# Performance work log

Hardware: AMD Instinct MI355X
Metric: run time of the kernel (lower is better)

## Reference

```python
import jax, jax.numpy as jnp
import numpy as np

D_MODEL = 1024
N_HEADS = 16
HEAD_DIM = D_MODEL // N_HEADS
B, T = 2, 2048

def setup_inputs() -> dict:
    key = jax.random.key(0)
    ks = jax.random.split(key, 9)
    s = 1.0 / np.sqrt(D_MODEL)
    return {
        "x": jax.random.normal(ks[0], (B, T, D_MODEL), dtype=jnp.float32),
        "Wq": jax.random.normal(ks[1], (D_MODEL, D_MODEL), dtype=jnp.float32) * s,
        "bq": jax.random.normal(ks[2], (D_MODEL,), dtype=jnp.float32) * 0.01,
        "Wk": jax.random.normal(ks[3], (D_MODEL, D_MODEL), dtype=jnp.float32) * s,
        "bk": jax.random.normal(ks[4], (D_MODEL,), dtype=jnp.float32) * 0.01,
        "Wv": jax.random.normal(ks[5], (D_MODEL, D_MODEL), dtype=jnp.float32) * s,
        "bv": jax.random.normal(ks[6], (D_MODEL,), dtype=jnp.float32) * 0.01,
        "Wo": jax.random.normal(ks[7], (D_MODEL, D_MODEL), dtype=jnp.float32) * s,
        "bo": jax.random.normal(ks[8], (D_MODEL,), dtype=jnp.float32) * 0.01,
    }

def reference(x, Wq, bq, Wk, bk, Wv, bv, Wo, bo):
    b, t, c = x.shape
    # Projections; reshape to [B, H, T, Dh]
    def heads(w, bias):
        return (x @ w.T + bias).reshape(b, t, N_HEADS, HEAD_DIM).transpose(0, 2, 1, 3)
    q = heads(Wq, bq)
    k = heads(Wk, bk)
    v = heads(Wv, bv)
    scale = 1.0 / np.sqrt(HEAD_DIM)
    att = jnp.einsum("bhqd,bhkd->bhqk", q, k) * scale  # [B,H,T,T]
    causal = jnp.tril(jnp.ones((t, t), dtype=bool))
    att = jnp.where(causal, att, -jnp.inf)
    att = jax.nn.softmax(att, axis=-1)
    # dropout p=0.0 (eval) -> identity
    y = jnp.einsum("bhqk,bhkd->bhqd", att, v)  # [B,H,T,Dh]
    y = y.transpose(0, 2, 1, 3).reshape(b, t, c)
    return y @ Wo.T + bo
```

## Files before the change

kernel.cpp:

```cpp
#include <hip/hip_runtime.h>
#include <stdint.h>


typedef unsigned short u16;
typedef __attribute__((ext_vector_type(8)))  __bf16 bf16x8;
typedef __attribute__((ext_vector_type(4)))  float  f32x4;
typedef __attribute__((ext_vector_type(16))) float  f32x16;
typedef __attribute__((ext_vector_type(4)))  float  float4v;
typedef __attribute__((ext_vector_type(4)))  unsigned short u16x4;
typedef __attribute__((ext_vector_type(4)))  unsigned int   u32x4;
typedef __attribute__((ext_vector_type(8)))  short  short8;

#define BB 2
#define TT 2048
#define DD 1024
#define HH 16
#define DH 64
#define MM (BB*TT)
#define NSLOT 1280
#define CEXP 0.18033688011f
#define XNE ((size_t)MM*DD)
#define WNE ((size_t)DD*DD)

static __device__ __forceinline__ u16 f2bf(float f) {
    uint32_t u = __builtin_bit_cast(uint32_t, f);
    u += 0x7FFFu + ((u >> 16) & 1u);
    return (u16)(u >> 16);
}
static __device__ __forceinline__ float bf2f(u16 v) {
    uint32_t u = (uint32_t)v << 16;
    return __builtin_bit_cast(float, u);
}

static __device__ __forceinline__ unsigned cvt_pk_bf16(float a, float b) {
    unsigned r;
    asm("v_cvt_pk_bf16_f32 %0, %1, %2" : "=v"(r) : "v"(a), "v"(b));
    return r;
}

static __device__ __forceinline__ void load_lds16(const u16* g, const u16* lds_base) {
    __builtin_amdgcn_global_load_lds(
        (const __attribute__((address_space(1))) void*)(uintptr_t)g,
        (__attribute__((address_space(3)))  void*)(uint32_t)(uintptr_t)lds_base,
        16u, 0, 0u);
}

static __device__ __forceinline__ f32x4 mfma16(bf16x8 a, bf16x8 b, f32x4 c) {
    return __builtin_amdgcn_mfma_f32_16x16x32_bf16(a, b, c, 0, 0, 0);
}
static __device__ __forceinline__ f32x16 mfma32(bf16x8 a, bf16x8 b, f32x16 c) {
    return __builtin_amdgcn_mfma_f32_32x32x16_bf16(a, b, c, 0, 0, 0);
}

static __device__ __forceinline__ float tree_sum16(const f32x16& a) {
    float m[8];
#pragma unroll
    for (int r = 0; r < 8; ++r) m[r] = a[r] + a[r + 8];
#pragma unroll
    for (int off = 4; off; off >>= 1)
#pragma unroll
        for (int r = 0; r < off; ++r) m[r] += m[r + off];
    return m[0];
}

static __device__ __forceinline__ bf16x8 pack8(float s0, float s1, float s2,
        float s3, float s4, float s5, float s6, float s7) {
    unsigned c0 = cvt_pk_bf16(s0, s1);
    unsigned c1 = cvt_pk_bf16(s2, s3);
    unsigned c2 = cvt_pk_bf16(s4, s5);
    unsigned c3 = cvt_pk_bf16(s6, s7);
    asm volatile("v_permlane32_swap_b32 %0, %1" : "+v"(c0), "+v"(c2));
    asm volatile("v_permlane32_swap_b32 %0, %1" : "+v"(c1), "+v"(c3));
    u32x4 w; w[0] = c0; w[1] = c1; w[2] = c2; w[3] = c3;
    return __builtin_bit_cast(bf16x8, w);
}

__global__ __launch_bounds__(256) void cvt_kernel(const float* __restrict__ src,
                                                  u16* __restrict__ dst, int n8) {
    int i = blockIdx.x * blockDim.x + threadIdx.x;
    int stride = gridDim.x * blockDim.x;
    for (; i < n8; i += stride) {
        float4v a = ((const float4v*)src)[2 * i];
        float4v b = ((const float4v*)src)[2 * i + 1];
        u32x4 o;
        o[0] = cvt_pk_bf16(a[0], a[1]); o[1] = cvt_pk_bf16(a[2], a[3]);
        o[2] = cvt_pk_bf16(b[0], b[1]); o[3] = cvt_pk_bf16(b[2], b[3]);
        ((u32x4*)dst)[i] = o;
    }
}

__global__ __launch_bounds__(256) void cvt4_kernel(const float* __restrict__ s0,
        const float* __restrict__ s1, const float* __restrict__ s2,
        const float* __restrict__ s3, u16* __restrict__ d0, u16* __restrict__ d1,
        u16* __restrict__ d2, u16* __restrict__ d3, int n8) {
    const int z = blockIdx.y;
    const float* src = (z == 0) ? s0 : (z == 1) ? s1 : (z == 2) ? s2 : s3;
    u16* dst = (z == 0) ? d0 : (z == 1) ? d1 : (z == 2) ? d2 : d3;
    const float sc = (z == 0) ? CEXP : 1.0f;
    int i = blockIdx.x * blockDim.x + threadIdx.x;
    int stride = gridDim.x * blockDim.x;
    for (; i < n8; i += stride) {
        float4v a = ((const float4v*)src)[2 * i];
        float4v b = ((const float4v*)src)[2 * i + 1];
        u32x4 o;
        o[0] = cvt_pk_bf16(a[0] * sc, a[1] * sc);
        o[1] = cvt_pk_bf16(a[2] * sc, a[3] * sc);
        o[2] = cvt_pk_bf16(b[0] * sc, b[1] * sc);
        o[3] = cvt_pk_bf16(b[2] * sc, b[3] * sc);
        ((u32x4*)dst)[i] = o;
    }
}

template<int MODE>
__global__ __launch_bounds__(256) void gemm2(const u16* __restrict__ xb,
        const u16* __restrict__ Wb, const float* __restrict__ bq,
        const float* __restrict__ bk, const float* __restrict__ bvv,
        u16* __restrict__ outq, u16* __restrict__ vt, float* __restrict__ outf) {
    __shared__ alignas(16) u16 As[2][128 * 32];
    __shared__ alignas(16) u16 Bs[2][128 * 32];

    const int tid  = threadIdx.x;
    const int wave = tid >> 6, lane = tid & 63;
    const int lr = lane & 15, lg = lane >> 4;
    const int wr = wave >> 1, wc = wave & 1;
    const int K = 1024;

    const u16 *Ap, *Wp;
    int m0, n0, zb = 0;
    bool vtmode = false;
    const int id = blockIdx.x;
    if (MODE == 0) {
        if (id < 512) {
            zb = id >> 8; int r = id & 255;
            m0 = (r >> 3) * 128; n0 = (r & 7) * 128;
            Ap = xb; Wp = Wb + (size_t)zb * WNE;
        } else {
            int v = id - 512; zb = v >> 7; int r = v & 127;
            m0 = (r >> 4) * 128; n0 = (r & 15) * 128;
            Ap = Wb + 2 * WNE;
            Wp = xb + (size_t)zb * 2048 * 1024;
            vtmode = true;
        }
    } else {
        m0 = (id >> 3) * 128; n0 = (id & 7) * 128;
        Ap = xb; Wp = Wb;
    }

    f32x4 acc[4][4];
#pragma unroll
    for (int m = 0; m < 4; ++m)
#pragma unroll
        for (int n = 0; n < 4; ++n) acc[m][n] = (f32x4){0.f, 0.f, 0.f, 0.f};

#define G_STAGE(BB_, KK_)                                                     \
    {                                                                         \
        _Pragma("unroll")                                                     \
        for (int it = 0; it < 2; ++it) {                                      \
            int c = it * 256 + tid;                                           \
            int row = c >> 2, cc = (c & 3) * 8;                               \
            load_lds16(Ap + (size_t)(m0 + row) * K + (KK_) + cc,              \
                       &As[BB_][(size_t)(it * 256 + wave * 64) * 8]);         \
            load_lds16(Wp + (size_t)(n0 + row) * K + (KK_) + cc,              \
                       &Bs[BB_][(size_t)(it * 256 + wave * 64) * 8]);         \
        }                                                                     \
    }

    G_STAGE(0, 0);
    __syncthreads();
    int cur = 0;
    for (int k0 = 0; k0 < K; k0 += 32) {
        if (k0 + 32 < K) G_STAGE(cur ^ 1, k0 + 32);

        bf16x8 af[4], bfm[4];
#pragma unroll
        for (int m = 0; m < 4; ++m)
            af[m] = *(const bf16x8*)&As[cur][(wr * 64 + m * 16 + lr) * 32 + lg * 8];
#pragma unroll
        for (int n = 0; n < 4; ++n)
            bfm[n] = *(const bf16x8*)&Bs[cur][(wc * 64 + n * 16 + lr) * 32 + lg * 8];
#pragma unroll
        for (int m = 0; m < 4; ++m)
#pragma unroll
            for (int n = 0; n < 4; ++n)
                acc[m][n] = mfma16(af[m], bfm[n], acc[m][n]);

        __syncthreads();
        cur ^= 1;
    }
#undef G_STAGE

    if (MODE == 1) {
#pragma unroll
        for (int n = 0; n < 4; ++n) {
            int col = n0 + wc * 64 + n * 16 + lr;
            float bvl = bq[col];
#pragma unroll
            for (int m = 0; m < 4; ++m) {
                int row = m0 + wr * 64 + m * 16 + lg * 4;
#pragma unroll
                for (int r = 0; r < 4; ++r)
                    outf[(size_t)(row + r) * 1024 + col] = acc[m][n][r] + bvl;
            }
        }
    } else if (!vtmode) {
        const float* bias = zb ? bk : bq;
        const float bsc = zb ? 1.0f : CEXP;
#pragma unroll
        for (int n = 0; n < 4; ++n) {
            int col = n0 + wc * 64 + n * 16 + lr;
            float bvl = bias[col] * bsc;
#pragma unroll
            for (int m = 0; m < 4; ++m) {
                int row = m0 + wr * 64 + m * 16 + lg * 4;
#pragma unroll
                for (int r = 0; r < 4; ++r)
                    outq[(size_t)zb * XNE + (size_t)(row + r) * 1024 + col] =
                        f2bf(acc[m][n][r] + bvl);
            }
        }
    } else {
        u16* vo = vt + (size_t)zb * 1024 * 2048;
#pragma unroll
        for (int m = 0; m < 4; ++m) {
            int rowb = m0 + wr * 64 + m * 16 + lg * 4;
            float bvr[4];
#pragma unroll
            for (int r = 0; r < 4; ++r) bvr[r] = bvv[rowb + r];
#pragma unroll
            for (int n = 0; n < 4; ++n) {
                int col = n0 + wc * 64 + n * 16 + lr;
#pragma unroll
                for (int r = 0; r < 4; ++r)
                    vo[(size_t)(rowb + r) * 2048 + col] = f2bf(acc[m][n][r] + bvr[r]);
            }
        }
    }
}

__global__ __launch_bounds__(256) void attn_part(const u16* __restrict__ Qb,
        const u16* __restrict__ Kb, const u16* __restrict__ VTb,
        u16* __restrict__ Op, float* __restrict__ Ml, u16* __restrict__ Yb) {
    __shared__ alignas(16) u16 Ks[64 * 64];
    __shared__ alignas(16) u16 Vs[64 * 64];

    const int tid  = threadIdx.x;
    const int wave = tid >> 6, lane = tid & 63;
    const int lq = lane & 31, hi = lane >> 5;

    const int i0 = blockIdx.x;
    const int bh = (i0 & 7) * 4 + ((i0 >> 3) / 40);
    const int s  = (i0 >> 3) % 40;
    int qi = 0, ch = 0;
    {
        int cum = 0, found = 0;
#pragma unroll
        for (int j = 0; j < 16; ++j) {
            int n = (j >> 2) + 1;
            if (!found && s < cum + n) { qi = j; ch = s - cum; found = 1; }
            cum += n;
        }
    }
    const int nc = (qi >> 2) + 1;
    const int b = bh >> 4, h = bh & 15;
    const size_t rb = (size_t)b * TT;
    const int hoff = h * DH;
    const int q0w = qi * 128 + wave * 32;
    const int k0 = ch * 512;
    const int kend = qi * 128 + 128;
    const int k1 = (k0 + 512 < kend) ? k0 + 512 : kend;

    const int srow0 = tid >> 3, sl = tid & 7;
    const int srow1 = (256 + tid) >> 3;

    const u16* Kbh = Kb + rb * DD + hoff;
    const u16* Vbh = VTb + (size_t)bh * 64 * 2048;

    bf16x8 qf[4];
    {
        const u16* qrow = Qb + (rb + q0w + lq) * DD + hoff + hi * 8;
#pragma unroll
        for (int kc = 0; kc < 4; ++kc) qf[kc] = *(const bf16x8*)(qrow + kc * 16);
    }

    f32x16 o0 = {}, o1 = {};
    float l_i = 0.f;

    for (int kv0 = k0; kv0 < k1; kv0 += 64) {
        __syncthreads();
        load_lds16(Kbh + (size_t)(kv0 + srow0) * DD + (sl ^ (srow0 & 7)) * 8,
                   &Ks[(size_t)(wave * 64) * 8]);
        load_lds16(Kbh + (size_t)(kv0 + srow1) * DD + (sl ^ (srow1 & 7)) * 8,
                   &Ks[(size_t)(256 + wave * 64) * 8]);
        load_lds16(Vbh + (size_t)srow0 * 2048 + kv0 + (sl ^ (srow0 & 7)) * 8,
                   &Vs[(size_t)(wave * 64) * 8]);
        load_lds16(Vbh + (size_t)srow1 * 2048 + kv0 + (sl ^ (srow1 & 7)) * 8,
                   &Vs[(size_t)(256 + wave * 64) * 8]);
        __syncthreads();

        if (kv0 < q0w + 32) {
            const int rowm = lq & 7;
            const bool diag = (kv0 + 63 > q0w);
            const int qrel = q0w + lq - kv0;
            bf16x8 pb[4];

            {
                f32x16 st = {};
#pragma unroll
                for (int kc = 0; kc < 4; ++kc) {
                    bf16x8 kf = *(const bf16x8*)&Ks[lq * 64 + ((2 * kc + hi) ^ rowm) * 8];
                    st = mfma32(kf, qf[kc], st);
                }
                if (diag) {
#pragma unroll
                    for (int r = 0; r < 16; ++r) {
                        int key = (r & 3) + 8 * (r >> 2) + 4 * hi;
                        if (key > qrel) st[r] = -1e30f;
                    }
                }
#pragma unroll
                for (int r = 0; r < 16; ++r) st[r] = __builtin_amdgcn_exp2f(st[r]);
                l_i += tree_sum16(st);
                pb[0] = pack8(st[0], st[1], st[2], st[3], st[4], st[5], st[6], st[7]);
                pb[1] = pack8(st[8], st[9], st[10], st[11], st[12], st[13], st[14], st[15]);
            }
            {
                f32x16 st = {};
#pragma unroll
                for (int kc = 0; kc < 4; ++kc) {
                    bf16x8 kf = *(const bf16x8*)&Ks[(32 + lq) * 64 + ((2 * kc + hi) ^ rowm) * 8];
                    st = mfma32(kf, qf[kc], st);
                }
                if (diag) {
#pragma unroll
                    for (int r = 0; r < 16; ++r) {
                        int key = 32 + (r & 3) + 8 * (r >> 2) + 4 * hi;
                        if (key > qrel) st[r] = -1e30f;
                    }
                }
#pragma unroll
                for (int r = 0; r < 16; ++r) st[r] = __builtin_amdgcn_exp2f(st[r]);
                l_i += tree_sum16(st);
                pb[2] = pack8(st[0], st[1], st[2], st[3], st[4], st[5], st[6], st[7]);
                pb[3] = pack8(st[8], st[9], st[10], st[11], st[12], st[13], st[14], st[15]);
            }

#pragma unroll
            for (int ks = 0; ks < 4; ++ks) {
                bf16x8 vf0 = *(const bf16x8*)&Vs[lq * 64        + ((ks * 2 + hi) ^ rowm) * 8];
                bf16x8 vf1 = *(const bf16x8*)&Vs[(32 + lq) * 64 + ((ks * 2 + hi) ^ rowm) * 8];
                o0 = mfma32(vf0, pb[ks], o0);
                o1 = mfma32(vf1, pb[ks], o1);
            }
        }
    }

    l_i += __shfl_xor(l_i, 32);
    const int col = wave * 32 + lq;

    if (nc == 1) {
        const float inv = 1.0f / l_i;
        u16* yrow = Yb + (rb + q0w + lq) * DD + hoff;
#pragma unroll
        for (int g = 0; g < 4; ++g) {
            u16x4 p0, p1;
#pragma unroll
            for (int j = 0; j < 4; ++j) {
                p0[j] = f2bf(o0[4 * g + j] * inv);
                p1[j] = f2bf(o1[4 * g + j] * inv);
            }
            *(u16x4*)&yrow[8 * g + 4 * hi]      = p0;
            *(u16x4*)&yrow[32 + 8 * g + 4 * hi] = p1;
        }
    } else {
        const int slot = bh * 40 + s;
        u16* op = Op + (size_t)slot * 8192;
#pragma unroll
        for (int r = 0; r < 16; ++r) {
            const int d0 = (r & 3) + 8 * (r >> 2) + 4 * hi;
            op[d0 * 128 + col]        = f2bf(o0[r]);
            op[(32 + d0) * 128 + col] = f2bf(o1[r]);
        }
        if (hi == 0) Ml[(size_t)slot * 128 + col] = l_i;
    }
}

__global__ __launch_bounds__(256) void attn_merge(const u16* __restrict__ Op,
        const float* __restrict__ Ml, u16* __restrict__ Yb) {
    const int bq = blockIdx.x;
    const int bh = bq >> 4, qi = bq & 15;
    const int nc = (qi >> 2) + 1;
    if (nc == 1) return;
    int cum = 0;
#pragma unroll
    for (int j = 0; j < 16; ++j) cum += (j < qi) ? ((j >> 2) + 1) : 0;
    const int s0 = bh * 40 + cum;

    const int t = threadIdx.x;
    const int row = t >> 1, dh = (t & 1) * 32;

    float L = 0.f;
    float acc[32];
#pragma unroll
    for (int d = 0; d < 32; ++d) acc[d] = 0.f;
#pragma unroll
    for (int c = 0; c < 4; ++c) {
        if (c < nc) {
            L += Ml[(size_t)(s0 + c) * 128 + row];
            const u16* op = Op + (size_t)(s0 + c) * 8192 + row;
#pragma unroll
            for (int d = 0; d < 32; ++d)
                acc[d] += bf2f(op[(dh + d) * 128]);
        }
    }
    const float inv = 1.0f / L;

    const int b = bh >> 4, h = bh & 15;
    u16* yrow = Yb + ((size_t)(b * TT + qi * 128 + row)) * DD + h * DH + dh;
#pragma unroll
    for (int g = 0; g < 8; ++g) {
        u16x4 p;
#pragma unroll
        for (int j = 0; j < 4; ++j) p[j] = f2bf(acc[4 * g + j] * inv);
        *(u16x4*)&yrow[4 * g] = p;
    }
}

extern "C" void kernel_launch(void* const* d_in, const int* in_sizes, int n_in,
                              void* d_out, int out_size, void* d_ws, size_t ws_size,
                              hipStream_t stream) {
    const float* x  = (const float*)d_in[0];
    const float* Wq = (const float*)d_in[1];
    const float* bq = (const float*)d_in[2];
    const float* Wk = (const float*)d_in[3];
    const float* bk = (const float*)d_in[4];
    const float* Wv = (const float*)d_in[5];
    const float* bv = (const float*)d_in[6];
    const float* Wo = (const float*)d_in[7];
    const float* bo = (const float*)d_in[8];
    float* out = (float*)d_out;

    u16* xb  = (u16*)d_ws;
    u16* Wb  = xb  + XNE;
    u16* Wob = Wb  + 3 * WNE;
    u16* QKV = Wob + WNE;
    u16* Yb  = QKV + 3 * XNE;
    u16* Op  = Yb  + XNE;
    float* Ml = (float*)(Op + (size_t)NSLOT * 8192);

    cvt_kernel<<<1024, 256, 0, stream>>>(x, xb, (int)(XNE / 8));
    cvt4_kernel<<<dim3(128, 4), 256, 0, stream>>>(Wq, Wk, Wv, Wo,
            Wb, Wb + WNE, Wb + 2 * WNE, Wob, (int)(WNE / 8));

    gemm2<0><<<768, 256, 0, stream>>>(xb, Wb, bq, bk, bv,
                                      QKV, QKV + 2 * XNE, nullptr);
    attn_part<<<NSLOT, 256, 0, stream>>>(QKV, QKV + XNE, QKV + 2 * XNE,
                                         Op, Ml, Yb);
    attn_merge<<<512, 256, 0, stream>>>(Op, Ml, Yb);
    gemm2<1><<<256, 256, 0, stream>>>(Yb, Wob, bo, nullptr, nullptr,
                                      nullptr, nullptr, out);
}
```

Before: 116.3 us.

## Double attention KV tile to 128 keys and merge conversion kernels into one launch

```diff
diff --git a/kernel.cpp b/kernel.cpp
--- a/kernel.cpp
+++ b/kernel.cpp
@@ -75,28 +75,21 @@
     return __builtin_bit_cast(bf16x8, w);
 }
 
-__global__ __launch_bounds__(256) void cvt_kernel(const float* __restrict__ src,
-                                                  u16* __restrict__ dst, int n8) {
-    int i = blockIdx.x * blockDim.x + threadIdx.x;
-    int stride = gridDim.x * blockDim.x;
-    for (; i < n8; i += stride) {
-        float4v a = ((const float4v*)src)[2 * i];
-        float4v b = ((const float4v*)src)[2 * i + 1];
-        u32x4 o;
-        o[0] = cvt_pk_bf16(a[0], a[1]); o[1] = cvt_pk_bf16(a[2], a[3]);
-        o[2] = cvt_pk_bf16(b[0], b[1]); o[3] = cvt_pk_bf16(b[2], b[3]);
-        ((u32x4*)dst)[i] = o;
-    }
-}
-
-__global__ __launch_bounds__(256) void cvt4_kernel(const float* __restrict__ s0,
-        const float* __restrict__ s1, const float* __restrict__ s2,
-        const float* __restrict__ s3, u16* __restrict__ d0, u16* __restrict__ d1,
-        u16* __restrict__ d2, u16* __restrict__ d3, int n8) {
-    const int z = blockIdx.y;
-    const float* src = (z == 0) ? s0 : (z == 1) ? s1 : (z == 2) ? s2 : s3;
-    u16* dst = (z == 0) ? d0 : (z == 1) ? d1 : (z == 2) ? d2 : d3;
-    const float sc = (z == 0) ? CEXP : 1.0f;
+__global__ __launch_bounds__(256) void cvt5_kernel(const float* __restrict__ x,
+        const float* __restrict__ w0, const float* __restrict__ w1,
+        const float* __restrict__ w2, const float* __restrict__ w3,
+        u16* __restrict__ xd, u16* __restrict__ d0, u16* __restrict__ d1,
+        u16* __restrict__ d2, u16* __restrict__ d3) {
+    const int y = blockIdx.y;
+    const float* src;
+    u16* dst;
+    float sc = 1.0f;
+    if (y < 4) { src = x + (size_t)y * (XNE / 4); dst = xd + (size_t)y * (XNE / 4); }
+    else if (y == 4) { src = w0; dst = d0; sc = CEXP; }
+    else if (y == 5) { src = w1; dst = d1; }
+    else if (y == 6) { src = w2; dst = d2; }
+    else            { src = w3; dst = d3; }
+    const int n8 = (int)(WNE / 8);
     int i = blockIdx.x * blockDim.x + threadIdx.x;
     int stride = gridDim.x * blockDim.x;
     for (; i < n8; i += stride) {
@@ -240,8 +233,8 @@
 __global__ __launch_bounds__(256) void attn_part(const u16* __restrict__ Qb,
         const u16* __restrict__ Kb, const u16* __restrict__ VTb,
         u16* __restrict__ Op, float* __restrict__ Ml, u16* __restrict__ Yb) {
-    __shared__ alignas(16) u16 Ks[64 * 64];
-    __shared__ alignas(16) u16 Vs[64 * 64];
+    __shared__ alignas(16) u16 Ks[128 * 64];
+    __shared__ alignas(16) u16 Vs[64 * 128];
 
     const int tid  = threadIdx.x;
     const int wave = tid >> 6, lane = tid & 63;
@@ -269,9 +262,6 @@
     const int kend = qi * 128 + 128;
     const int k1 = (k0 + 512 < kend) ? k0 + 512 : kend;
 
-    const int srow0 = tid >> 3, sl = tid & 7;
-    const int srow1 = (256 + tid) >> 3;
-
     const u16* Kbh = Kb + rb * DD + hoff;
     const u16* Vbh = VTb + (size_t)bh * 64 * 2048;
 
@@ -284,72 +274,86 @@
 
     f32x16 o0 = {}, o1 = {};
     float l_i = 0.f;
-
-    for (int kv0 = k0; kv0 < k1; kv0 += 64) {
+    const int rowm = lq & 7;
+
+    for (int kv0 = k0; kv0 < k1; kv0 += 128) {
         __syncthreads();
-        load_lds16(Kbh + (size_t)(kv0 + srow0) * DD + (sl ^ (srow0 & 7)) * 8,
-                   &Ks[(size_t)(wave * 64) * 8]);
-        load_lds16(Kbh + (size_t)(kv0 + srow1) * DD + (sl ^ (srow1 & 7)) * 8,
-                   &Ks[(size_t)(256 + wave * 64) * 8]);
-        load_lds16(Vbh + (size_t)srow0 * 2048 + kv0 + (sl ^ (srow0 & 7)) * 8,
-                   &Vs[(size_t)(wave * 64) * 8]);
-        load_lds16(Vbh + (size_t)srow1 * 2048 + kv0 + (sl ^ (srow1 & 7)) * 8,
-                   &Vs[(size_t)(256 + wave * 64) * 8]);
+#pragma unroll
+        for (int it = 0; it < 4; ++it) {
+            int c = it * 256 + tid;
+            int krow = c >> 3, ksl = c & 7;
+            load_lds16(Kbh + (size_t)(kv0 + krow) * DD + ((ksl ^ (krow & 7)) * 8),
+                       &Ks[(size_t)(it * 256 + wave * 64) * 8]);
+        }
+#pragma unroll
+        for (int it = 0; it < 4; ++it) {
+            int c = it * 256 + tid;
+            int vrow = c >> 4, vsl = c & 15;
+            load_lds16(Vbh + (size_t)vrow * 2048 + kv0 + ((vsl ^ (vrow & 7)) * 8),
+                       &Vs[(size_t)(it * 256 + wave * 64) * 8]);
+        }
         __syncthreads();
 
-        if (kv0 < q0w + 32) {
-            const int rowm = lq & 7;
-            const bool diag = (kv0 + 63 > q0w);
-            const int qrel = q0w + lq - kv0;
-            bf16x8 pb[4];
-
-            {
-                f32x16 st = {};
-#pragma unroll
-                for (int kc = 0; kc < 4; ++kc) {
-                    bf16x8 kf = *(const bf16x8*)&Ks[lq * 64 + ((2 * kc + hi) ^ rowm) * 8];
-                    st = mfma32(kf, qf[kc], st);
+#pragma unroll
+        for (int sub = 0; sub < 2; ++sub) {
+            const int kb = kv0 + sub * 64;
+            if (kb < q0w + 32) {
+                const bool diag = (kb + 63 > q0w);
+                const int qrel = q0w + lq - kb;
+                bf16x8 pb[4];
+
+                {
+                    f32x16 st = {};
+#pragma unroll
+                    for (int kc = 0; kc < 4; ++kc) {
+                        bf16x8 kf = *(const bf16x8*)&Ks[(sub * 64 + lq) * 64 +
+                                                        ((2 * kc + hi) ^ rowm) * 8];
+                        st = mfma32(kf, qf[kc], st);
+                    }
+                    if (diag) {
+#pragma unroll
+                        for (int r = 0; r < 16; ++r) {
+                            int key = (r & 3) + 8 * (r >> 2) + 4 * hi;
+                            if (key > qrel) st[r] = -1e30f;
+                        }
+                    }
+#pragma unroll
+                    for (int r = 0; r < 16; ++r) st[r] = __builtin_amdgcn_exp2f(st[r]);
+                    l_i += tree_sum16(st);
+                    pb[0] = pack8(st[0], st[1], st[2], st[3], st[4], st[5], st[6], st[7]);
+                    pb[1] = pack8(st[8], st[9], st[10], st[11], st[12], st[13], st[14], st[15]);
                 }
-                if (diag) {
-#pragma unroll
-                    for (int r = 0; r < 16; ++r) {
-                        int key = (r & 3) + 8 * (r >> 2) + 4 * hi;
-                        if (key > qrel) st[r] = -1e30f;
+                {
+                    f32x16 st = {};
+#pragma unroll
+                    for (int kc = 0; kc < 4; ++kc) {
+                        bf16x8 kf = *(const bf16x8*)&Ks[(sub * 64 + 32 + lq) * 64 +
+                                                        ((2 * kc + hi) ^ rowm) * 8];
+                        st = mfma32(kf, qf[kc], st);
                     }
+                    if (diag) {
+#pragma unroll
+                        for (int r = 0; r < 16; ++r) {
+                            int key = 32 + (r & 3) + 8 * (r >> 2) + 4 * hi;
+                            if (key > qrel) st[r] = -1e30f;
+                        }
+                    }
+#pragma unroll
+                    for (int r = 0; r < 16; ++r) st[r] = __builtin_amdgcn_exp2f(st[r]);
+                    l_i += tree_sum16(st);
+                    pb[2] = pack8(st[0], st[1], st[2], st[3], st[4], st[5], st[6], st[7]);
+                    pb[3] = pack8(st[8], st[9], st[10], st[11], st[12], st[13], st[14], st[15]);
                 }
-#pragma unroll
-                for (int r = 0; r < 16; ++r) st[r] = __builtin_amdgcn_exp2f(st[r]);
-                l_i += tree_sum16(st);
-                pb[0] = pack8(st[0], st[1], st[2], st[3], st[4], st[5], st[6], st[7]);
-                pb[1] = pack8(st[8], st[9], st[10], st[11], st[12], st[13], st[14], st[15]);
-            }
-            {
-                f32x16 st = {};
-#pragma unroll
-                for (int kc = 0; kc < 4; ++kc) {
-                    bf16x8 kf = *(const bf16x8*)&Ks[(32 + lq) * 64 + ((2 * kc + hi) ^ rowm) * 8];
-                    st = mfma32(kf, qf[kc], st);
+
+#pragma unroll
+                for (int ks = 0; ks < 4; ++ks) {
+                    bf16x8 vf0 = *(const bf16x8*)&Vs[lq * 128 +
+                                    (sub * 8 + ((ks * 2 + hi) ^ rowm)) * 8];
+                    bf16x8 vf1 = *(const bf16x8*)&Vs[(32 + lq) * 128 +
+                                    (sub * 8 + ((ks * 2 + hi) ^ rowm)) * 8];
+                    o0 = mfma32(vf0, pb[ks], o0);
+                    o1 = mfma32(vf1, pb[ks], o1);
                 }
-                if (diag) {
-#pragma unroll
-                    for (int r = 0; r < 16; ++r) {
-                        int key = 32 + (r & 3) + 8 * (r >> 2) + 4 * hi;
-                        if (key > qrel) st[r] = -1e30f;
-                    }
-                }
-#pragma unroll
-                for (int r = 0; r < 16; ++r) st[r] = __builtin_amdgcn_exp2f(st[r]);
-                l_i += tree_sum16(st);
-                pb[2] = pack8(st[0], st[1], st[2], st[3], st[4], st[5], st[6], st[7]);
-                pb[3] = pack8(st[8], st[9], st[10], st[11], st[12], st[13], st[14], st[15]);
-            }
-
-#pragma unroll
-            for (int ks = 0; ks < 4; ++ks) {
-                bf16x8 vf0 = *(const bf16x8*)&Vs[lq * 64        + ((ks * 2 + hi) ^ rowm) * 8];
-                bf16x8 vf1 = *(const bf16x8*)&Vs[(32 + lq) * 64 + ((ks * 2 + hi) ^ rowm) * 8];
-                o0 = mfma32(vf0, pb[ks], o0);
-                o1 = mfma32(vf1, pb[ks], o1);
             }
         }
     }
@@ -447,9 +451,8 @@
     u16* Op  = Yb  + XNE;
     float* Ml = (float*)(Op + (size_t)NSLOT * 8192);
 
-    cvt_kernel<<<1024, 256, 0, stream>>>(x, xb, (int)(XNE / 8));
-    cvt4_kernel<<<dim3(128, 4), 256, 0, stream>>>(Wq, Wk, Wv, Wo,
-            Wb, Wb + WNE, Wb + 2 * WNE, Wob, (int)(WNE / 8));
+    cvt5_kernel<<<dim3(128, 8), 256, 0, stream>>>(x, Wq, Wk, Wv, Wo,
+            xb, Wb, Wb + WNE, Wb + 2 * WNE, Wob);
 
     gemm2<0><<<768, 256, 0, stream>>>(xb, Wb, bq, bk, bv,
                                       QKV, QKV + 2 * XNE, nullptr);
```

After: 114.8 us. Within noise of the previous version (-1.3%).
